# Performance work log

Measured on AMD Instinct MI355X. Metric: run time of the kernel, lower is better.

The kernel has to match this reference:

```python
import jax, jax.numpy as jnp
import numpy as np

T, H, E, K = 16384, 2880, 128, 4

def setup_inputs() -> dict:
    key = jax.random.key(0)
    k1, k2, k3 = jax.random.split(key, 3)
    return {
        "hidden_states": jax.random.normal(k1, (T, H), dtype=jnp.float32),
        "weight": jax.random.normal(k2, (E, H), dtype=jnp.float32) * 0.02,
        "bias": jax.random.normal(k3, (E,), dtype=jnp.float32) * 0.02,
    }

def reference(hidden_states, weight, bias):
    x = hidden_states.reshape(-1, weight.shape[1])            # [T, H]
    logits = jnp.einsum('th,eh->te', x, weight) + bias        # [T, E]
    top_val, top_idx = jax.lax.top_k(logits, K)               # sorted desc, [T, K]
    top_val = jax.nn.softmax(top_val, axis=-1)
    rows = jnp.arange(logits.shape[0])[:, None]
    scores = jnp.zeros_like(logits).at[rows, top_idx].set(top_val)
    return scores, top_idx
```

## Files before the change

### kernel.cpp

```cpp
#include <hip/hip_runtime.h>
#include <math.h>


#define T_TOK 16384
#define HDIM  2880
#define EEXP  128
#define KTOP  4

#define TM   32
#define NT   256
#define KC   64
#define NCH  (HDIM / KC)
#define XBUF 8192
#define TAU  2.5e-4f

typedef __attribute__((ext_vector_type(8))) short bf16x8;
typedef __attribute__((ext_vector_type(4))) float f32x4;

#define MFMA(a, b, c) __builtin_amdgcn_mfma_f32_16x16x32_bf16((a), (b), (c), 0, 0, 0)

__global__ __launch_bounds__(256) void w_split(
    const float* __restrict__ w, char* __restrict__ wp)
{
    const int gid  = blockIdx.x * 256 + threadIdx.x;
    const int lane = gid & 63;
    const int q    = gid >> 6;
    const int ks   = q & 1;
    const int q2   = q >> 1;
    const int c    = q2 % NCH;
    const int F    = q2 / NCH;
    const int e    = F * 16 + (lane & 15);
    const int k0   = c * 64 + ks * 32 + (lane >> 4) * 8;

    const float* src = w + (size_t)e * HDIM + k0;
    float4 v0 = *(const float4*)(src);
    float4 v1 = *(const float4*)(src + 4);
    float vv[8] = {v0.x, v0.y, v0.z, v0.w, v1.x, v1.y, v1.z, v1.w};
    union { unsigned short s[8]; uint4 u; } H, L;
#pragma unroll
    for (int j = 0; j < 8; ++j) {
        unsigned u = __float_as_uint(vv[j]);
        H.s[j] = (unsigned short)(u >> 16);
        float rr = vv[j] - __uint_as_float(u & 0xffff0000u);
        L.s[j] = (unsigned short)(__float_as_uint(rr) >> 16);
    }
    const int tile = ((F * NCH + c) * 2 + ks) * 2;
    *(uint4*)(wp + (size_t)tile * 1024 + lane * 16)       = H.u;
    *(uint4*)(wp + (size_t)(tile + 1) * 1024 + lane * 16) = L.u;
}

static __device__ __forceinline__ void split_write256(char* base, int off, float4 v) {
    union { float4 v4; unsigned u[4]; } uv; uv.v4 = v;
    unsigned h01 = __builtin_amdgcn_perm(uv.u[1], uv.u[0], 0x07060302u);
    unsigned h23 = __builtin_amdgcn_perm(uv.u[3], uv.u[2], 0x07060302u);
    float r0 = v.x - __uint_as_float(uv.u[0] & 0xffff0000u);
    float r1 = v.y - __uint_as_float(uv.u[1] & 0xffff0000u);
    float r2 = v.z - __uint_as_float(uv.u[2] & 0xffff0000u);
    float r3 = v.w - __uint_as_float(uv.u[3] & 0xffff0000u);
    unsigned l01 = __builtin_amdgcn_perm(__float_as_uint(r1), __float_as_uint(r0), 0x07060302u);
    unsigned l23 = __builtin_amdgcn_perm(__float_as_uint(r3), __float_as_uint(r2), 0x07060302u);
    uint2 hw; hw.x = h01; hw.y = h23;
    uint2 lw; lw.x = l01; lw.y = l23;
    *(uint2*)(base + off)       = hw;
    *(uint2*)(base + off + 128) = lw;
}

__global__ __launch_bounds__(NT, 2) void router_fused(
    const float* __restrict__ x, const char* __restrict__ wp,
    const float* __restrict__ w, const float* __restrict__ bias,
    float* __restrict__ out)
{
    __shared__ char smem[20480];
    const int tid  = threadIdx.x;
    const int tok0 = blockIdx.x * TM;
    const int lane = tid & 63;
    const int wv   = tid >> 6;
    const int r    = lane & 15;
    const int g    = lane >> 4;

    char* xb0 = smem;
    char* xb1 = smem + XBUF;

    int xoff[2];
    const float* xptr[2];
#pragma unroll
    for (int i = 0; i < 2; ++i) {
        int f = tid + i * NT;
        int row = f >> 4, c4 = f & 15;
        xoff[i] = row * 256 + ((((c4 >> 1) ^ (row & 7)) << 4) | ((c4 & 1) << 3));
        xptr[i] = x + (size_t)(tok0 + row) * HDIM + c4 * 4;
    }

    int aoff[2][2];
#pragma unroll
    for (int tf = 0; tf < 2; ++tf) {
        int row = tf * 16 + r;
#pragma unroll
        for (int ks = 0; ks < 2; ++ks)
            aoff[tf][ks] = row * 256 + (((ks * 4 + g) ^ (row & 7)) << 4);
    }

    f32x4 a00 = {0.f, 0.f, 0.f, 0.f}, a01 = a00, a10 = a00, a11 = a00;

#define LOADX(pf, cc) do {                                            \
        pf[0] = *(const float4*)(xptr[0] + (cc) * KC);                \
        pf[1] = *(const float4*)(xptr[1] + (cc) * KC); } while (0)

#define WRITEX(pf, bb) do {                                           \
        split_write256((bb), xoff[0], pf[0]);                         \
        split_write256((bb), xoff[1], pf[1]); } while (0)

#define LOADW(W, cc) do {                                             \
        _Pragma("unroll")                                             \
        for (int F2 = 0; F2 < 2; ++F2)                                \
        _Pragma("unroll")                                             \
        for (int ks_ = 0; ks_ < 2; ++ks_)                             \
        _Pragma("unroll")                                             \
        for (int p_ = 0; p_ < 2; ++p_)                                \
            W[F2*4 + ks_*2 + p_] = *(const bf16x8*)(wp +              \
                (size_t)((((wv*2 + F2) * NCH + (cc)) * 2 + ks_) * 2 + p_) * 1024 \
                + lane * 16); } while (0)

#define MFMA_CHUNK(cb, W) do {                                        \
        _Pragma("unroll")                                             \
        for (int ks_ = 0; ks_ < 2; ++ks_) {                           \
            bf16x8 ah0 = *(const bf16x8*)((cb) + aoff[0][ks_]);       \
            bf16x8 al0 = *(const bf16x8*)((cb) + aoff[0][ks_] + 128); \
            bf16x8 ah1 = *(const bf16x8*)((cb) + aoff[1][ks_]);       \
            bf16x8 al1 = *(const bf16x8*)((cb) + aoff[1][ks_] + 128); \
            bf16x8 bh0 = W[ks_*2],     bl0 = W[ks_*2 + 1];            \
            bf16x8 bh1 = W[4 + ks_*2], bl1 = W[4 + ks_*2 + 1];        \
            a00 = MFMA(ah0, bh0, a00); a01 = MFMA(ah0, bh1, a01);     \
            a10 = MFMA(ah1, bh0, a10); a11 = MFMA(ah1, bh1, a11);     \
            a00 = MFMA(ah0, bl0, a00); a01 = MFMA(ah0, bl1, a01);     \
            a10 = MFMA(ah1, bl0, a10); a11 = MFMA(ah1, bl1, a11);     \
            a00 = MFMA(al0, bh0, a00); a01 = MFMA(al0, bh1, a01);     \
            a10 = MFMA(al1, bh0, a10); a11 = MFMA(al1, bh1, a11);     \
        } } while (0)

    float4 pf[2];
    bf16x8 wA[8], wB[8];

    LOADX(pf, 0);
    LOADW(wA, 0);
    WRITEX(pf, xb0);
    __syncthreads();

    for (int c = 0; c < NCH - 1; c += 2) {
        LOADX(pf, c + 1); LOADW(wB, c + 1);
        MFMA_CHUNK(xb0, wA);
        WRITEX(pf, xb1);
        __syncthreads();
        if (c + 2 < NCH) { LOADX(pf, c + 2); LOADW(wA, c + 2); }
        MFMA_CHUNK(xb1, wB);
        if (c + 2 < NCH) WRITEX(pf, xb0);
        __syncthreads();
    }
    MFMA_CHUNK(xb0, wA);
    __syncthreads();

    float* logitsL = (float*)smem;
    const float bv0 = bias[wv * 32 + r];
    const float bv1 = bias[wv * 32 + 16 + r];
#pragma unroll
    for (int q = 0; q < 4; ++q) {
        int m0 = g * 4 + q, m1 = m0 + 16;
        int e0 = wv * 32 + r, e1 = e0 + 16;
        logitsL[m0 * 130 + e0] = a00[q] + bv0;
        logitsL[m0 * 130 + e1] = a01[q] + bv1;
        logitsL[m1 * 130 + e0] = a10[q] + bv0;
        logitsL[m1 * 130 + e1] = a11[q] + bv1;
    }
    float*  cvf = (float*) (smem + 16640);
    int*    cie = (int*)   (smem + 17664);
    int*    flg = (int*)   (smem + 18688);
    double* svd = (double*)(smem + 18816);
    int*    sid = (int*)   (smem + 19840);
    double* cvd = (double*)(smem + 20352);
    __syncthreads();

    {
        const int t = tid >> 3, s = tid & 7;
        float v[8]; int id[8];
#pragma unroll
        for (int k = 0; k < 8; ++k) { v[k] = -3.4e38f; id[k] = 0x7fffffff; }
        for (int jj = 0; jj < 16; ++jj) {
            float lv = logitsL[t * 130 + s * 16 + jj];
            int   e  = s * 16 + jj;
            bool gt[8];
#pragma unroll
            for (int k = 0; k < 8; ++k)
                gt[k] = (lv > v[k]) || (lv == v[k] && e < id[k]);
#pragma unroll
            for (int k = 7; k >= 1; --k)
                if (gt[k - 1]) { v[k] = v[k - 1]; id[k] = id[k - 1]; }
#pragma unroll
            for (int k = 0; k < 8; ++k) {
                bool put = gt[k] && (k == 0 || !gt[k - 1]);
                if (put) { v[k] = lv; id[k] = e; }
            }
        }
#pragma unroll
        for (int rd = 0; rd < 8; ++rd) {
            float hv = v[0]; int hi = id[0];
#pragma unroll
            for (int off = 1; off < 8; off <<= 1) {
                float ov = __shfl_xor(hv, off);
                int   oi = __shfl_xor(hi, off);
                if (ov > hv || (ov == hv && oi < hi)) { hv = ov; hi = oi; }
            }
            if (s == 0) { cvf[t * 8 + rd] = hv; cie[t * 8 + rd] = hi; }
            bool mine = (v[0] == hv) && (id[0] == hi);
            if (mine) {
#pragma unroll
                for (int k = 0; k < 7; ++k) { v[k] = v[k + 1]; id[k] = id[k + 1]; }
                v[7] = -3.4e38f; id[7] = 0x7fffffff;
            }
        }
    }
    __syncthreads();

    if (tid < TM) {
        float gmin = 3.4e38f;
#pragma unroll
        for (int k = 0; k < 4; ++k)
            gmin = fminf(gmin, cvf[tid * 8 + k] - cvf[tid * 8 + k + 1]);
        flg[tid] = (gmin < TAU);
    }
    if (tid < 128) {
        int t2 = tid >> 2, k = tid & 3;
        svd[t2 * 4 + k] = (double)cvf[t2 * 8 + k];
        sid[t2 * 4 + k] = cie[t2 * 8 + k];
    }
    __syncthreads();

    for (int ts = 0; ts < TM; ++ts) {
        if (!flg[ts]) continue;
#pragma unroll
        for (int h2 = 0; h2 < 2; ++h2) {
            const int cand = wv * 2 + h2;
            const int ce = cie[ts * 8 + cand];
            const float4* xr = (const float4*)(x + (size_t)(tok0 + ts) * HDIM);
            const float4* wr = (const float4*)(w + (size_t)ce * HDIM);
            double q0 = 0.0, q1 = 0.0, q2 = 0.0, q3 = 0.0;
            for (int i2 = 0; i2 < 12; ++i2) {
                int fi = lane + i2 * 64;
                if (fi < HDIM / 4) {
                    float4 xv = xr[fi];
                    float4 wv4 = wr[fi];
                    q0 = fma((double)xv.x, (double)wv4.x, q0);
                    q1 = fma((double)xv.y, (double)wv4.y, q1);
                    q2 = fma((double)xv.z, (double)wv4.z, q2);
                    q3 = fma((double)xv.w, (double)wv4.w, q3);
                }
            }
            double accd = (q0 + q2) + (q1 + q3);
#pragma unroll
            for (int off = 32; off > 0; off >>= 1)
                accd += __shfl_xor(accd, off);
            if (lane == 0) cvd[cand] = accd + (double)bias[ce];
        }
        __syncthreads();
        if (tid < 8) {
            double mv = cvd[tid]; int mi2 = cie[ts * 8 + tid];
            int rk = 0;
#pragma unroll
            for (int j2 = 0; j2 < 8; ++j2) {
                double oj = cvd[j2];
                rk += (oj > mv) || (oj == mv && cie[ts * 8 + j2] < mi2);
            }
            if (rk < 4) { svd[ts * 4 + rk] = mv; sid[ts * 4 + rk] = mi2; }
        }
        __syncthreads();
    }

    float* srow = (float*)smem;
    float4 z4 = make_float4(0.f, 0.f, 0.f, 0.f);
#pragma unroll
    for (int i = 0; i < 4; ++i)
        ((float4*)srow)[tid + i * NT] = z4;
    __syncthreads();

    if (tid < TM) {
        double m  = svd[tid * 4];
        double e0 = exp(svd[tid * 4 + 0] - m), e1 = exp(svd[tid * 4 + 1] - m);
        double e2 = exp(svd[tid * 4 + 2] - m), e3 = exp(svd[tid * 4 + 3] - m);
        double inv = 1.0 / ((e0 + e1) + (e2 + e3));
        float* oidx = out + (size_t)T_TOK * EEXP + (size_t)(tok0 + tid) * KTOP;
        int i0 = sid[tid * 4 + 0], i1 = sid[tid * 4 + 1];
        int i2 = sid[tid * 4 + 2], i3 = sid[tid * 4 + 3];
        oidx[0] = (float)i0; oidx[1] = (float)i1;
        oidx[2] = (float)i2; oidx[3] = (float)i3;
        srow[tid * EEXP + i0] = (float)(e0 * inv);
        srow[tid * EEXP + i1] = (float)(e1 * inv);
        srow[tid * EEXP + i2] = (float)(e2 * inv);
        srow[tid * EEXP + i3] = (float)(e3 * inv);
    }
    __syncthreads();

    float4* orow = (float4*)(out + (size_t)tok0 * EEXP);
#pragma unroll
    for (int i = 0; i < 4; ++i)
        orow[tid + i * NT] = ((float4*)srow)[tid + i * NT];
}

extern "C" void kernel_launch(void* const* d_in, const int* in_sizes, int n_in,
                              void* d_out, int out_size, void* d_ws, size_t ws_size,
                              hipStream_t stream) {
    const float* x    = (const float*)d_in[0];
    const float* w    = (const float*)d_in[1];
    const float* bias = (const float*)d_in[2];
    float* out        = (float*)d_out;
    char*  wp         = (char*)d_ws;

    hipLaunchKernelGGL(w_split, dim3(180), dim3(256), 0, stream, w, wp);
    hipLaunchKernelGGL(router_fused, dim3(T_TOK / TM), dim3(NT), 0, stream,
                       x, wp, w, bias, out);
}
```

Measured before the change: 85.09 us.

## Triple-buffer X chunks with deeper register prefetch in router GEMM loop

After: 80.22 us. 1.06x faster.

```diff
diff --git a/kernel.cpp b/kernel.cpp
--- a/kernel.cpp
+++ b/kernel.cpp
@@ -70,7 +70,7 @@
     const float* __restrict__ w, const float* __restrict__ bias,
     float* __restrict__ out)
 {
-    __shared__ char smem[20480];
+    __shared__ char smem[3 * XBUF];
     const int tid  = threadIdx.x;
     const int tok0 = blockIdx.x * TM;
     const int lane = tid & 63;
@@ -80,6 +80,7 @@
 
     char* xb0 = smem;
     char* xb1 = smem + XBUF;
+    char* xb2 = smem + 2 * XBUF;
 
     int xoff[2];
     const float* xptr[2];
@@ -138,26 +139,31 @@
             a10 = MFMA(al1, bh0, a10); a11 = MFMA(al1, bh1, a11);     \
         } } while (0)
 
-    float4 pf[2];
-    bf16x8 wA[8], wB[8];
-
-    LOADX(pf, 0);
-    LOADW(wA, 0);
-    WRITEX(pf, xb0);
-    __syncthreads();
-
-    for (int c = 0; c < NCH - 1; c += 2) {
-        LOADX(pf, c + 1); LOADW(wB, c + 1);
+    float4 pfA[2], pfB[2], pfC[2];
+    bf16x8 wA[8], wB[8], wC[8];
+
+    LOADX(pfA, 0); LOADX(pfB, 1); LOADX(pfC, 2);
+    LOADW(wA, 0); LOADW(wB, 1);
+    WRITEX(pfA, xb0);
+    __syncthreads();
+
+    for (int c = 0; c < NCH; c += 3) {
+        if (c + 3 < NCH) LOADX(pfA, c + 3);
+        LOADW(wC, c + 2);
         MFMA_CHUNK(xb0, wA);
-        WRITEX(pf, xb1);
-        __syncthreads();
-        if (c + 2 < NCH) { LOADX(pf, c + 2); LOADW(wA, c + 2); }
+        WRITEX(pfB, xb1);
+        __syncthreads();
+        if (c + 3 < NCH) LOADW(wA, c + 3);
+        if (c + 4 < NCH) LOADX(pfB, c + 4);
         MFMA_CHUNK(xb1, wB);
-        if (c + 2 < NCH) WRITEX(pf, xb0);
-        __syncthreads();
-    }
-    MFMA_CHUNK(xb0, wA);
-    __syncthreads();
+        WRITEX(pfC, xb2);
+        __syncthreads();
+        if (c + 4 < NCH) LOADW(wB, c + 4);
+        if (c + 5 < NCH) LOADX(pfC, c + 5);
+        MFMA_CHUNK(xb2, wC);
+        if (c + 3 < NCH) WRITEX(pfA, xb0);
+        __syncthreads();
+    }
 
     float* logitsL = (float*)smem;
     const float bv0 = bias[wv * 32 + r];
```

## Split K across two warp groups with 512-thread blocks and larger chunks

Applied to the files above, without the earlier changes.

New measurement: 81.67 us. 1.04x faster.

```diff
diff --git a/kernel.cpp b/kernel.cpp
--- a/kernel.cpp
+++ b/kernel.cpp
@@ -7,12 +7,12 @@
 #define EEXP  128
 #define KTOP  4
 
-#define TM   32
-#define NT   256
-#define KC   64
-#define NCH  (HDIM / KC)
-#define XBUF 8192
-#define TAU  2.5e-4f
+#define TM    32
+#define NT    512
+#define KCH   96
+#define NPH   15
+#define HALFK 1440
+#define TAU   2.5e-4f
 
 typedef __attribute__((ext_vector_type(8))) short bf16x8;
 typedef __attribute__((ext_vector_type(4))) float f32x4;
@@ -25,12 +25,10 @@
     const int gid  = blockIdx.x * 256 + threadIdx.x;
     const int lane = gid & 63;
     const int q    = gid >> 6;
-    const int ks   = q & 1;
-    const int q2   = q >> 1;
-    const int c    = q2 % NCH;
-    const int F    = q2 / NCH;
+    const int c32  = q % 90;
+    const int F    = q / 90;
     const int e    = F * 16 + (lane & 15);
-    const int k0   = c * 64 + ks * 32 + (lane >> 4) * 8;
+    const int k0   = c32 * 32 + (lane >> 4) * 8;
 
     const float* src = w + (size_t)e * HDIM + k0;
     float4 v0 = *(const float4*)(src);
@@ -44,12 +42,12 @@
         float rr = vv[j] - __uint_as_float(u & 0xffff0000u);
         L.s[j] = (unsigned short)(__float_as_uint(rr) >> 16);
     }
-    const int tile = ((F * NCH + c) * 2 + ks) * 2;
+    const int tile = (F * 90 + c32) * 2;
     *(uint4*)(wp + (size_t)tile * 1024 + lane * 16)       = H.u;
     *(uint4*)(wp + (size_t)(tile + 1) * 1024 + lane * 16) = L.u;
 }
 
-static __device__ __forceinline__ void split_write256(char* base, int off, float4 v) {
+static __device__ __forceinline__ void split_write(char* base, int off, float4 v) {
     union { float4 v4; unsigned u[4]; } uv; uv.v4 = v;
     unsigned h01 = __builtin_amdgcn_perm(uv.u[1], uv.u[0], 0x07060302u);
     unsigned h23 = __builtin_amdgcn_perm(uv.u[3], uv.u[2], 0x07060302u);
@@ -62,74 +60,83 @@
     uint2 hw; hw.x = h01; hw.y = h23;
     uint2 lw; lw.x = l01; lw.y = l23;
     *(uint2*)(base + off)       = hw;
-    *(uint2*)(base + off + 128) = lw;
+    *(uint2*)(base + off + 256) = lw;
 }
 
-__global__ __launch_bounds__(NT, 2) void router_fused(
+__global__ __launch_bounds__(NT, 4) void router_fused(
     const float* __restrict__ x, const char* __restrict__ wp,
     const float* __restrict__ w, const float* __restrict__ bias,
     float* __restrict__ out)
 {
-    __shared__ char smem[20480];
+    __shared__ char smem[65536];
     const int tid  = threadIdx.x;
     const int tok0 = blockIdx.x * TM;
     const int lane = tid & 63;
     const int wv   = tid >> 6;
+    const int kt   = wv >> 2;
+    const int wn   = wv & 3;
     const int r    = lane & 15;
     const int g    = lane >> 4;
 
-    char* xb0 = smem;
-    char* xb1 = smem + XBUF;
-
-    int xoff[2];
-    const float* xptr[2];
-#pragma unroll
-    for (int i = 0; i < 2; ++i) {
-        int f = tid + i * NT;
-        int row = f >> 4, c4 = f & 15;
-        xoff[i] = row * 256 + ((((c4 >> 1) ^ (row & 7)) << 4) | ((c4 & 1) << 3));
-        xptr[i] = x + (size_t)(tok0 + row) * HDIM + c4 * 4;
-    }
-
-    int aoff[2][2];
+    int hoff[3];
+    const float* xptr[3];
+#pragma unroll
+    for (int i = 0; i < 3; ++i) {
+        int f    = tid + i * NT;
+        int half = (f >= 768) ? 1 : 0;
+        int ff   = f - half * 768;
+        int row  = ff / 24, c4 = ff % 24;
+        int s    = c4 >> 1;
+        hoff[i] = half * 32768 + row * 512 +
+                  (((s ^ (row & 7)) << 4) | ((c4 & 1) << 3));
+        xptr[i] = x + (size_t)(tok0 + row) * HDIM + half * HALFK + c4 * 4;
+    }
+
+    int aoff[2][3];
 #pragma unroll
     for (int tf = 0; tf < 2; ++tf) {
         int row = tf * 16 + r;
 #pragma unroll
-        for (int ks = 0; ks < 2; ++ks)
-            aoff[tf][ks] = row * 256 + (((ks * 4 + g) ^ (row & 7)) << 4);
+        for (int ks = 0; ks < 3; ++ks) {
+            int s = ks * 4 + g;
+            aoff[tf][ks] = kt * 32768 + row * 512 + (((s ^ (row & 7)) << 4));
+        }
     }
 
     f32x4 a00 = {0.f, 0.f, 0.f, 0.f}, a01 = a00, a10 = a00, a11 = a00;
 
 #define LOADX(pf, cc) do {                                            \
-        pf[0] = *(const float4*)(xptr[0] + (cc) * KC);                \
-        pf[1] = *(const float4*)(xptr[1] + (cc) * KC); } while (0)
-
-#define WRITEX(pf, bb) do {                                           \
-        split_write256((bb), xoff[0], pf[0]);                         \
-        split_write256((bb), xoff[1], pf[1]); } while (0)
+        pf[0] = *(const float4*)(xptr[0] + (cc) * KCH);               \
+        pf[1] = *(const float4*)(xptr[1] + (cc) * KCH);               \
+        pf[2] = *(const float4*)(xptr[2] + (cc) * KCH); } while (0)
+
+#define WRITEX(pf, cc) do { int bo_ = ((cc) & 1) * 16384;             \
+        split_write(smem, hoff[0] + bo_, pf[0]);                      \
+        split_write(smem, hoff[1] + bo_, pf[1]);                      \
+        split_write(smem, hoff[2] + bo_, pf[2]); } while (0)
 
 #define LOADW(W, cc) do {                                             \
         _Pragma("unroll")                                             \
-        for (int F2 = 0; F2 < 2; ++F2)                                \
+        for (int ks_ = 0; ks_ < 3; ++ks_)                             \
         _Pragma("unroll")                                             \
-        for (int ks_ = 0; ks_ < 2; ++ks_)                             \
+        for (int F2_ = 0; F2_ < 2; ++F2_)                             \
         _Pragma("unroll")                                             \
-        for (int p_ = 0; p_ < 2; ++p_)                                \
-            W[F2*4 + ks_*2 + p_] = *(const bf16x8*)(wp +              \
-                (size_t)((((wv*2 + F2) * NCH + (cc)) * 2 + ks_) * 2 + p_) * 1024 \
-                + lane * 16); } while (0)
-
-#define MFMA_CHUNK(cb, W) do {                                        \
+        for (int p_ = 0; p_ < 2; ++p_) {                              \
+            int c32_ = kt * 45 + (cc) * 3 + ks_;                      \
+            int tile_ = ((wn * 2 + F2_) * 90 + c32_) * 2 + p_;        \
+            W[ks_*4 + F2_*2 + p_] = *(const bf16x8*)(wp +             \
+                (size_t)tile_ * 1024 + lane * 16);                    \
+        } } while (0)
+
+#define MFMA_CHUNK(bo, W) do {                                        \
         _Pragma("unroll")                                             \
-        for (int ks_ = 0; ks_ < 2; ++ks_) {                           \
-            bf16x8 ah0 = *(const bf16x8*)((cb) + aoff[0][ks_]);       \
-            bf16x8 al0 = *(const bf16x8*)((cb) + aoff[0][ks_] + 128); \
-            bf16x8 ah1 = *(const bf16x8*)((cb) + aoff[1][ks_]);       \
-            bf16x8 al1 = *(const bf16x8*)((cb) + aoff[1][ks_] + 128); \
-            bf16x8 bh0 = W[ks_*2],     bl0 = W[ks_*2 + 1];            \
-            bf16x8 bh1 = W[4 + ks_*2], bl1 = W[4 + ks_*2 + 1];        \
+        for (int ks_ = 0; ks_ < 3; ++ks_) {                           \
+            bf16x8 ah0 = *(const bf16x8*)(smem + aoff[0][ks_] + (bo));\
+            bf16x8 al0 = *(const bf16x8*)(smem + aoff[0][ks_] + (bo) + 256);\
+            bf16x8 ah1 = *(const bf16x8*)(smem + aoff[1][ks_] + (bo));\
+            bf16x8 al1 = *(const bf16x8*)(smem + aoff[1][ks_] + (bo) + 256);\
+            bf16x8 bh0 = W[ks_*4], bl0 = W[ks_*4+1];                  \
+            bf16x8 bh1 = W[ks_*4+2], bl1 = W[ks_*4+3];                \
             a00 = MFMA(ah0, bh0, a00); a01 = MFMA(ah0, bh1, a01);     \
             a10 = MFMA(ah1, bh0, a10); a11 = MFMA(ah1, bh1, a11);     \
             a00 = MFMA(ah0, bl0, a00); a01 = MFMA(ah0, bl1, a01);     \
@@ -138,48 +145,66 @@
             a10 = MFMA(al1, bh0, a10); a11 = MFMA(al1, bh1, a11);     \
         } } while (0)
 
-    float4 pf[2];
-    bf16x8 wA[8], wB[8];
-
-    LOADX(pf, 0);
-    LOADW(wA, 0);
-    WRITEX(pf, xb0);
-    __syncthreads();
-
-    for (int c = 0; c < NCH - 1; c += 2) {
-        LOADX(pf, c + 1); LOADW(wB, c + 1);
-        MFMA_CHUNK(xb0, wA);
-        WRITEX(pf, xb1);
+    float4 pfA[3], pfB[3];
+    bf16x8 W[12];
+
+    LOADX(pfA, 0); LOADX(pfB, 1);
+    WRITEX(pfA, 0);
+    LOADX(pfA, 2);
+    __syncthreads();
+
+    for (int c = 0; c < 14; c += 2) {
+        WRITEX(pfB, c + 1);
+        if (c + 3 < NPH) LOADX(pfB, c + 3);
+        LOADW(W, c);
+        MFMA_CHUNK(0, W);
         __syncthreads();
-        if (c + 2 < NCH) { LOADX(pf, c + 2); LOADW(wA, c + 2); }
-        MFMA_CHUNK(xb1, wB);
-        if (c + 2 < NCH) WRITEX(pf, xb0);
+        WRITEX(pfA, c + 2);
+        if (c + 4 < NPH) LOADX(pfA, c + 4);
+        LOADW(W, c + 1);
+        MFMA_CHUNK(16384, W);
         __syncthreads();
     }
-    MFMA_CHUNK(xb0, wA);
-    __syncthreads();
-
-    float* logitsL = (float*)smem;
-    const float bv0 = bias[wv * 32 + r];
-    const float bv1 = bias[wv * 32 + 16 + r];
-#pragma unroll
-    for (int q = 0; q < 4; ++q) {
-        int m0 = g * 4 + q, m1 = m0 + 16;
-        int e0 = wv * 32 + r, e1 = e0 + 16;
-        logitsL[m0 * 130 + e0] = a00[q] + bv0;
-        logitsL[m0 * 130 + e1] = a01[q] + bv1;
-        logitsL[m1 * 130 + e0] = a10[q] + bv0;
-        logitsL[m1 * 130 + e1] = a11[q] + bv1;
-    }
-    float*  cvf = (float*) (smem + 16640);
-    int*    cie = (int*)   (smem + 17664);
-    int*    flg = (int*)   (smem + 18688);
-    double* svd = (double*)(smem + 18816);
-    int*    sid = (int*)   (smem + 19840);
-    double* cvd = (double*)(smem + 20352);
-    __syncthreads();
-
-    {
+    LOADW(W, 14);
+    MFMA_CHUNK(0, W);
+    __syncthreads();
+
+    float* red = (float*)smem;
+    if (kt == 1) {
+#pragma unroll
+        for (int q = 0; q < 4; ++q) {
+            int t0 = g * 4 + q, t1 = t0 + 16;
+            red[(wn * 32 + t0) * 32 + r]      = a00[q];
+            red[(wn * 32 + t0) * 32 + 16 + r] = a01[q];
+            red[(wn * 32 + t1) * 32 + r]      = a10[q];
+            red[(wn * 32 + t1) * 32 + 16 + r] = a11[q];
+        }
+    }
+    __syncthreads();
+
+    float* logitsL = (float*)(smem + 16384);
+    if (kt == 0) {
+        const float bv0 = bias[wn * 32 + r];
+        const float bv1 = bias[wn * 32 + 16 + r];
+#pragma unroll
+        for (int q = 0; q < 4; ++q) {
+            int t0 = g * 4 + q, t1 = t0 + 16;
+            int e0 = wn * 32 + r, e1 = e0 + 16;
+            logitsL[t0 * 130 + e0] = a00[q] + red[(wn * 32 + t0) * 32 + r]      + bv0;
+            logitsL[t0 * 130 + e1] = a01[q] + red[(wn * 32 + t0) * 32 + 16 + r] + bv1;
+            logitsL[t1 * 130 + e0] = a10[q] + red[(wn * 32 + t1) * 32 + r]      + bv0;
+            logitsL[t1 * 130 + e1] = a11[q] + red[(wn * 32 + t1) * 32 + 16 + r] + bv1;
+        }
+    }
+    float*  cvf = (float*) (smem + 33024);
+    int*    cie = (int*)   (smem + 34048);
+    int*    flg = (int*)   (smem + 35072);
+    double* svd = (double*)(smem + 35200);
+    int*    sid = (int*)   (smem + 36224);
+    double* cvd = (double*)(smem + 36736);
+    __syncthreads();
+
+    if (tid < 256) {
         const int t = tid >> 3, s = tid & 7;
         float v[8]; int id[8];
 #pragma unroll
@@ -236,10 +261,8 @@
 
     for (int ts = 0; ts < TM; ++ts) {
         if (!flg[ts]) continue;
-#pragma unroll
-        for (int h2 = 0; h2 < 2; ++h2) {
-            const int cand = wv * 2 + h2;
-            const int ce = cie[ts * 8 + cand];
+        {
+            const int ce = cie[ts * 8 + wv];
             const float4* xr = (const float4*)(x + (size_t)(tok0 + ts) * HDIM);
             const float4* wr = (const float4*)(w + (size_t)ce * HDIM);
             double q0 = 0.0, q1 = 0.0, q2 = 0.0, q3 = 0.0;
@@ -258,7 +281,7 @@
 #pragma unroll
             for (int off = 32; off > 0; off >>= 1)
                 accd += __shfl_xor(accd, off);
-            if (lane == 0) cvd[cand] = accd + (double)bias[ce];
+            if (lane == 0) cvd[wv] = accd + (double)bias[ce];
         }
         __syncthreads();
         if (tid < 8) {
@@ -277,7 +300,7 @@
     float* srow = (float*)smem;
     float4 z4 = make_float4(0.f, 0.f, 0.f, 0.f);
 #pragma unroll
-    for (int i = 0; i < 4; ++i)
+    for (int i = 0; i < 2; ++i)
         ((float4*)srow)[tid + i * NT] = z4;
     __syncthreads();
 
@@ -300,7 +323,7 @@
 
     float4* orow = (float4*)(out + (size_t)tok0 * EEXP);
 #pragma unroll
-    for (int i = 0; i < 4; ++i)
+    for (int i = 0; i < 2; ++i)
         orow[tid + i * NT] = ((float4*)srow)[tid + i * NT];
 }
 
```

## Stream x tiles via global_load_lds into 4-stage ring; split bf16 after LDS read

Applied to the files above, without the earlier changes.

After: 87.01 us. 1.02x slower.

```diff
diff --git a/kernel.cpp b/kernel.cpp
--- a/kernel.cpp
+++ b/kernel.cpp
@@ -10,7 +10,7 @@
 #define TM   32
 #define NT   256
 #define KC   64
-#define NCH  (HDIM / KC)
+#define NCH  45
 #define XBUF 8192
 #define TAU  2.5e-4f
 
@@ -18,6 +18,10 @@
 typedef __attribute__((ext_vector_type(4))) float f32x4;
 
 #define MFMA(a, b, c) __builtin_amdgcn_mfma_f32_16x16x32_bf16((a), (b), (c), 0, 0, 0)
+
+#define GLL(g, l) __builtin_amdgcn_global_load_lds(                        \
+        (__attribute__((address_space(1))) void*)(g),                      \
+        (__attribute__((address_space(3))) void*)(l), 16, 0, 0)
 
 __global__ __launch_bounds__(256) void w_split(
     const float* __restrict__ w, char* __restrict__ wp)
@@ -49,20 +53,27 @@
     *(uint4*)(wp + (size_t)(tile + 1) * 1024 + lane * 16) = L.u;
 }
 
-static __device__ __forceinline__ void split_write256(char* base, int off, float4 v) {
-    union { float4 v4; unsigned u[4]; } uv; uv.v4 = v;
-    unsigned h01 = __builtin_amdgcn_perm(uv.u[1], uv.u[0], 0x07060302u);
-    unsigned h23 = __builtin_amdgcn_perm(uv.u[3], uv.u[2], 0x07060302u);
-    float r0 = v.x - __uint_as_float(uv.u[0] & 0xffff0000u);
-    float r1 = v.y - __uint_as_float(uv.u[1] & 0xffff0000u);
-    float r2 = v.z - __uint_as_float(uv.u[2] & 0xffff0000u);
-    float r3 = v.w - __uint_as_float(uv.u[3] & 0xffff0000u);
-    unsigned l01 = __builtin_amdgcn_perm(__float_as_uint(r1), __float_as_uint(r0), 0x07060302u);
-    unsigned l23 = __builtin_amdgcn_perm(__float_as_uint(r3), __float_as_uint(r2), 0x07060302u);
-    uint2 hw; hw.x = h01; hw.y = h23;
-    uint2 lw; lw.x = l01; lw.y = l23;
-    *(uint2*)(base + off)       = hw;
-    *(uint2*)(base + off + 128) = lw;
+static __device__ __forceinline__ void split8(float4 v0, float4 v1,
+                                              bf16x8* h8, bf16x8* l8) {
+    union { float4 f; unsigned u[4]; } a, b; a.f = v0; b.f = v1;
+    union { unsigned u[4]; bf16x8 v; } H, L;
+    H.u[0] = __builtin_amdgcn_perm(a.u[1], a.u[0], 0x07060302u);
+    H.u[1] = __builtin_amdgcn_perm(a.u[3], a.u[2], 0x07060302u);
+    H.u[2] = __builtin_amdgcn_perm(b.u[1], b.u[0], 0x07060302u);
+    H.u[3] = __builtin_amdgcn_perm(b.u[3], b.u[2], 0x07060302u);
+    float r0 = v0.x - __uint_as_float(a.u[0] & 0xffff0000u);
+    float r1 = v0.y - __uint_as_float(a.u[1] & 0xffff0000u);
+    float r2 = v0.z - __uint_as_float(a.u[2] & 0xffff0000u);
+    float r3 = v0.w - __uint_as_float(a.u[3] & 0xffff0000u);
+    float r4 = v1.x - __uint_as_float(b.u[0] & 0xffff0000u);
+    float r5 = v1.y - __uint_as_float(b.u[1] & 0xffff0000u);
+    float r6 = v1.z - __uint_as_float(b.u[2] & 0xffff0000u);
+    float r7 = v1.w - __uint_as_float(b.u[3] & 0xffff0000u);
+    L.u[0] = __builtin_amdgcn_perm(__float_as_uint(r1), __float_as_uint(r0), 0x07060302u);
+    L.u[1] = __builtin_amdgcn_perm(__float_as_uint(r3), __float_as_uint(r2), 0x07060302u);
+    L.u[2] = __builtin_amdgcn_perm(__float_as_uint(r5), __float_as_uint(r4), 0x07060302u);
+    L.u[3] = __builtin_amdgcn_perm(__float_as_uint(r7), __float_as_uint(r6), 0x07060302u);
+    *h8 = H.v; *l8 = L.v;
 }
 
 __global__ __launch_bounds__(NT, 2) void router_fused(
@@ -70,7 +81,7 @@
     const float* __restrict__ w, const float* __restrict__ bias,
     float* __restrict__ out)
 {
-    __shared__ char smem[20480];
+    __shared__ char smem[32768];
     const int tid  = threadIdx.x;
     const int tok0 = blockIdx.x * TM;
     const int lane = tid & 63;
@@ -78,37 +89,31 @@
     const int r    = lane & 15;
     const int g    = lane >> 4;
 
-    char* xb0 = smem;
-    char* xb1 = smem + XBUF;
-
-    int xoff[2];
-    const float* xptr[2];
-#pragma unroll
-    for (int i = 0; i < 2; ++i) {
-        int f = tid + i * NT;
-        int row = f >> 4, c4 = f & 15;
-        xoff[i] = row * 256 + ((((c4 >> 1) ^ (row & 7)) << 4) | ((c4 & 1) << 3));
-        xptr[i] = x + (size_t)(tok0 + row) * HDIM + c4 * 4;
-    }
-
-    int aoff[2][2];
+    const int m0 = wv * 2, m1 = wv * 2 + 1;
+    const int sr0 = m0 * 4 + (lane >> 4);
+    const int sr1 = m1 * 4 + (lane >> 4);
+    const float* gp0 = x + (size_t)(tok0 + sr0) * HDIM + (((lane & 15) ^ (sr0 & 7)) << 2);
+    const float* gp1 = x + (size_t)(tok0 + sr1) * HDIM + (((lane & 15) ^ (sr1 & 7)) << 2);
+    char* lbs0 = smem + m0 * 1024;
+    char* lbs1 = smem + m1 * 1024;
+
+    int aof[2][2][2];
 #pragma unroll
     for (int tf = 0; tf < 2; ++tf) {
         int row = tf * 16 + r;
 #pragma unroll
         for (int ks = 0; ks < 2; ++ks)
-            aoff[tf][ks] = row * 256 + (((ks * 4 + g) ^ (row & 7)) << 4);
+#pragma unroll
+            for (int j = 0; j < 2; ++j)
+                aof[tf][ks][j] = row * 256 + (((ks * 8 + g * 2 + j) ^ (r & 7)) << 4);
     }
 
     f32x4 a00 = {0.f, 0.f, 0.f, 0.f}, a01 = a00, a10 = a00, a11 = a00;
 
-#define LOADX(pf, cc) do {                                            \
-        pf[0] = *(const float4*)(xptr[0] + (cc) * KC);                \
-        pf[1] = *(const float4*)(xptr[1] + (cc) * KC); } while (0)
-
-#define WRITEX(pf, bb) do {                                           \
-        split_write256((bb), xoff[0], pf[0]);                         \
-        split_write256((bb), xoff[1], pf[1]); } while (0)
+#define ISSUEX(cc, bi) do {                                           \
+        GLL(gp0 + (size_t)(cc) * KC, lbs0 + (bi) * XBUF);             \
+        GLL(gp1 + (size_t)(cc) * KC, lbs1 + (bi) * XBUF);             \
+    } while (0)
 
 #define LOADW(W, cc) do {                                             \
         _Pragma("unroll")                                             \
@@ -121,13 +126,16 @@
                 (size_t)((((wv*2 + F2) * NCH + (cc)) * 2 + ks_) * 2 + p_) * 1024 \
                 + lane * 16); } while (0)
 
-#define MFMA_CHUNK(cb, W) do {                                        \
+#define MFMA_CHUNK(bp, W) do {                                        \
         _Pragma("unroll")                                             \
         for (int ks_ = 0; ks_ < 2; ++ks_) {                           \
-            bf16x8 ah0 = *(const bf16x8*)((cb) + aoff[0][ks_]);       \
-            bf16x8 al0 = *(const bf16x8*)((cb) + aoff[0][ks_] + 128); \
-            bf16x8 ah1 = *(const bf16x8*)((cb) + aoff[1][ks_]);       \
-            bf16x8 al1 = *(const bf16x8*)((cb) + aoff[1][ks_] + 128); \
+            float4 xv00 = *(const float4*)((bp) + aof[0][ks_][0]);    \
+            float4 xv01 = *(const float4*)((bp) + aof[0][ks_][1]);    \
+            float4 xv10 = *(const float4*)((bp) + aof[1][ks_][0]);    \
+            float4 xv11 = *(const float4*)((bp) + aof[1][ks_][1]);    \
+            bf16x8 ah0, al0, ah1, al1;                                \
+            split8(xv00, xv01, &ah0, &al0);                           \
+            split8(xv10, xv11, &ah1, &al1);                           \
             bf16x8 bh0 = W[ks_*2],     bl0 = W[ks_*2 + 1];            \
             bf16x8 bh1 = W[4 + ks_*2], bl1 = W[4 + ks_*2 + 1];        \
             a00 = MFMA(ah0, bh0, a00); a01 = MFMA(ah0, bh1, a01);     \
@@ -138,25 +146,29 @@
             a10 = MFMA(al1, bh0, a10); a11 = MFMA(al1, bh1, a11);     \
         } } while (0)
 
-    float4 pf[2];
+#define PHASE(cc, bi_rd, WC, WN) do {                                 \
+        asm volatile("s_waitcnt vmcnt(12)" ::: "memory");             \
+        __builtin_amdgcn_sched_barrier(0);                            \
+        __builtin_amdgcn_s_barrier();                                 \
+        __builtin_amdgcn_sched_barrier(0);                            \
+        if ((cc) + 3 < NCH) ISSUEX((cc) + 3, ((cc) + 3) & 3);         \
+        if ((cc) + 1 < NCH) LOADW(WN, (cc) + 1);                      \
+        MFMA_CHUNK(smem + (bi_rd) * XBUF, WC);                        \
+    } while (0)
+
     bf16x8 wA[8], wB[8];
 
-    LOADX(pf, 0);
+    ISSUEX(0, 0); ISSUEX(1, 1); ISSUEX(2, 2);
     LOADW(wA, 0);
-    WRITEX(pf, xb0);
-    __syncthreads();
-
-    for (int c = 0; c < NCH - 1; c += 2) {
-        LOADX(pf, c + 1); LOADW(wB, c + 1);
-        MFMA_CHUNK(xb0, wA);
-        WRITEX(pf, xb1);
-        __syncthreads();
-        if (c + 2 < NCH) { LOADX(pf, c + 2); LOADW(wA, c + 2); }
-        MFMA_CHUNK(xb1, wB);
-        if (c + 2 < NCH) WRITEX(pf, xb0);
-        __syncthreads();
-    }
-    MFMA_CHUNK(xb0, wA);
+
+    for (int it = 0; it < 11; ++it) {
+        int c = it * 4;
+        PHASE(c + 0, 0, wA, wB);
+        PHASE(c + 1, 1, wB, wA);
+        PHASE(c + 2, 2, wA, wB);
+        PHASE(c + 3, 3, wB, wA);
+    }
+    PHASE(44, 0, wA, wB);
     __syncthreads();
 
     float* logitsL = (float*)smem;
@@ -164,12 +176,12 @@
     const float bv1 = bias[wv * 32 + 16 + r];
 #pragma unroll
     for (int q = 0; q < 4; ++q) {
-        int m0 = g * 4 + q, m1 = m0 + 16;
+        int m0q = g * 4 + q, m1q = m0q + 16;
         int e0 = wv * 32 + r, e1 = e0 + 16;
-        logitsL[m0 * 130 + e0] = a00[q] + bv0;
-        logitsL[m0 * 130 + e1] = a01[q] + bv1;
-        logitsL[m1 * 130 + e0] = a10[q] + bv0;
-        logitsL[m1 * 130 + e1] = a11[q] + bv1;
+        logitsL[m0q * 130 + e0] = a00[q] + bv0;
+        logitsL[m0q * 130 + e1] = a01[q] + bv1;
+        logitsL[m1q * 130 + e0] = a10[q] + bv0;
+        logitsL[m1q * 130 + e1] = a11[q] + bv1;
     }
     float*  cvf = (float*) (smem + 16640);
     int*    cie = (int*)   (smem + 17664);
```
